# Kernel tuning notes

Measured on AMD Instinct MI355X. Metric: run time of the kernel, lower is better.

Reference implementation:

```python
import jax, jax.numpy as jnp
import numpy as np
import math

SQRT2 = float(np.sqrt(2.0))
INV_SQRT_2PI = float(1.0 / np.sqrt(2.0 * np.pi))


def _trunc_prob(x, mu, sigma):
    # Faithful port of TruncNormal.prob with a=-10, b=10
    a, b = -10.0, 10.0
    phi_b = 0.5 * (1.0 + jax.scipy.special.erf((b - mu) / sigma / SQRT2))
    phi_a = 0.5 * (1.0 + jax.scipy.special.erf((a - mu) / sigma / SQRT2))
    xs = jnp.where(x > b, x + 100.0, x)
    xs = jnp.where(xs < a, xs - 100.0, xs)
    xn = (xs - mu) / sigma
    dens = jnp.exp(-0.5 * xn * xn) * INV_SQRT_2PI
    dens = jnp.where((xn > b) | (xn < a), 0.0, dens)
    return dens / (phi_b - phi_a) + 1e-10


def _S_single(zg, tt, Wx, bx, Wt, bt, Wt2, bt2, Wf, bf, Wo, bo):
    # One tiny MLP applied to one group-slice zg (shape [g]) at scalar time tt.
    g = Wx.shape[0]
    x = jnp.tanh(Wx @ zg + bx)
    half = g // 2
    freqs = jnp.exp(jnp.arange(half, dtype=zg.dtype) * (-math.log(10000.0) / half))
    te = tt * freqs
    temb = jnp.concatenate([jnp.sin(te), jnp.cos(te)])  # [g]
    tv = jax.nn.gelu(Wt @ temb + bt, approximate=False)  # torch nn.GELU (exact)
    tv = Wt2 @ tv + bt2
    h = jnp.tanh(Wf @ (x + tv) + bf)
    return jnp.tanh(Wo @ h + bo)[0]  # scalar S


def _derivs(zg, tt, Wx, bx, Wt, bt, Wt2, bt2, Wf, bf, Wo, bo):
    p = (Wx, bx, Wt, bt, Wt2, bt2, Wf, bf, Wo, bo)
    f = lambda z_, t_: _S_single(z_, t_, *p)
    S = f(zg, tt)
    s_z = jax.grad(f, 0)(zg, tt)                    # dS/dz         [g]
    H = jax.jacfwd(jax.grad(f, 0), 0)(zg, tt)       # H[j,k]=d2S/dzj dzk  [g,g]
    dSdt = jax.grad(f, 1)(zg, tt)                   # dS/dt scalar
    return S, s_z, H, dSdt


def reference(z, time_step, mu, sigma, Wx, bx, Wt, bt, Wt2, bt2, Wf, bf, Wo, bo, beta):
    G, g = Wx.shape[0], Wx.shape[1]
    B = z.shape[0]
    tt = time_step[0]

    sig2 = sigma ** 2 + 1e-5
    nlp = -(z - mu) / sig2                                   # nabla_log_phi [B,n_in]
    dlp = -1.0 / sig2                                        # delta_log_phi (scalar-ish)
    dpp = ((z - mu) ** 2 - sigma ** 2) / (sigma ** 4 + 1e-5)  # delta_phi_over_phi
    rho = _trunc_prob(z, mu, sigma)

    to_g = lambda a: a.reshape(B, G, g).transpose(1, 0, 2)   # [G,B,g]
    zr, nlp_r, dpp_r, rho_r = to_g(z), to_g(nlp), to_g(dpp), to_g(rho)

    over_b = jax.vmap(_derivs, in_axes=(0, None) + (None,) * 10)
    over_g = jax.vmap(over_b, in_axes=(0, None) + (0,) * 10)
    S, s_z, H, dSdt = over_g(zr, tt, Wx, bx, Wt, bt, Wt2, bt2, Wf, bf, Wo, bo)
    # S [G,B], s_z [G,B,g], H [G,B,g,g], dSdt [G,B]

    bb = beta.reshape(G, 1, 1)
    u = S[..., None] - bb * jnp.log(jnp.prod(rho_r, axis=2, keepdims=True))  # [G,B,1]
    u_z = s_z - bb * nlp_r                                                    # [G,B,g]
    # torch grad(S.sum(), t): t is a single shared (1,1) tensor -> gradient sums over batch
    dSdt_sum = dSdt.sum(axis=1).reshape(G, 1, 1)
    # grad((rho*u_z).sum(), z_temp): rho and nabla_log_phi are constants wrt z_temp,
    # so gradient = sum_j rho_j * H[j,k]
    corr = jnp.einsum('gbj,gbjk->gbk', rho_r, H)
    u_t = dSdt_sum + bb * corr / (rho_r + 1e-5)
    # grad(s_z.sum(), z_temp)[k] = sum_j H[j,k]
    u_zz = H.sum(axis=2) - bb * dlp
    pde = u_t + 0.5 * u_z ** 2 + 0.125 * bb ** 2 * (nlp_r ** 2 - 2.0 * dpp_r)

    to_bn = lambda a: a.transpose(1, 0, 2).reshape(B, -1)
    return to_bn(pde), to_bn(u_z), u[:, :, 0].transpose(1, 0), to_bn(u_zz)


def setup_inputs() -> dict:
    B, N_IN, g = 8192, 512, 4
    G = N_IN // g
    key = jax.random.key(0)
    ks = jax.random.split(key, 16)

    def lin_w(k, fo, fi):
        return (jax.random.normal(k, (G, fo, fi), jnp.float32) / np.sqrt(fi)).astype(jnp.float32)

    def lin_b(k, fo):
        return (0.01 * jax.random.normal(k, (G, fo), jnp.float32)).astype(jnp.float32)

    return {
        "z": jax.random.normal(ks[0], (B, N_IN), jnp.float32),
        "time_step": jnp.ones((1,), jnp.float32),
        "mu": jnp.zeros((1,), jnp.float32),
        "sigma": jnp.ones((1,), jnp.float32),
        "Wx": lin_w(ks[1], g, g), "bx": lin_b(ks[2], g),
        "Wt": lin_w(ks[3], g, g), "bt": lin_b(ks[4], g),
        "Wt2": lin_w(ks[5], g, g), "bt2": lin_b(ks[6], g),
        "Wf": lin_w(ks[7], g, g), "bf": lin_b(ks[8], g),
        "Wo": lin_w(ks[9], 1, g), "bo": lin_b(ks[10], 1),
        "beta": jnp.ones((G, 1), jnp.float32),
    }
```

## Files before the change

kernel.cpp:

```cpp
#include <hip/hip_runtime.h>
#include <math.h>

#define NG 128
#define NIN 512
#define OFF1 4194304
#define OFF2 8388608
#define OFF3 9437184

#define INV_SQRT_2PI 0.3989422804014327f
#define INV_SQRT2    0.7071067811865476f

__device__ __forceinline__ float gelu_f(float x){
    return 0.5f*x*(1.0f + erff(x*INV_SQRT2));
}
__device__ __forceinline__ float gelu_df(float x){
    return 0.5f*(1.0f + erff(x*INV_SQRT2)) + x*INV_SQRT_2PI*expf(-0.5f*x*x);
}

__global__ void k_pre(const float* __restrict__ ts,
                      const float* __restrict__ Wt,  const float* __restrict__ bt,
                      const float* __restrict__ Wt2, const float* __restrict__ bt2,
                      float* __restrict__ tv_ws, float* __restrict__ dtv_ws){
    int g = threadIdx.x;
    if (g >= NG) return;
    float t  = ts[0];
    float f1 = expf(-0.5f*logf(10000.0f));
    float te0 = t, te1 = t*f1;
    float temb[4]  = { sinf(te0),  sinf(te1),     cosf(te0),     cosf(te1) };
    float dtemb[4] = { cosf(te0),  f1*cosf(te1), -sinf(te0), -f1*sinf(te1) };
    float tg[4], dg[4];
    #pragma unroll
    for (int i=0;i<4;i++){
        float a = bt[g*4+i], d = 0.0f;
        #pragma unroll
        for (int j=0;j<4;j++){
            float w = Wt[g*16+i*4+j];
            a += w*temb[j]; d += w*dtemb[j];
        }
        tg[i] = gelu_f(a);
        dg[i] = gelu_df(a)*d;
    }
    #pragma unroll
    for (int j=0;j<4;j++){
        float a = bt2[g*4+j], d = 0.0f;
        #pragma unroll
        for (int i=0;i<4;i++){
            float w = Wt2[g*16+j*4+i];
            a += w*tg[i]; d += w*dg[i];
        }
        tv_ws[g*4+j]  = a;
        dtv_ws[g*4+j] = d;
    }
}

__global__ __launch_bounds__(256) void k_dsdt(const float* __restrict__ z,
    const float* __restrict__ Wx, const float* __restrict__ bx,
    const float* __restrict__ Wf, const float* __restrict__ bf,
    const float* __restrict__ Wo, const float* __restrict__ bo,
    const float* __restrict__ tv_ws, const float* __restrict__ dtv_ws,
    float* __restrict__ partial){
    const int tid  = threadIdx.x;
    const int gidx = tid & 127;
    const int lb   = tid >> 7;
    float wx[16], wf[16];
    #pragma unroll
    for (int i=0;i<4;i++){
        float4 a4 = ((const float4*)(Wx + gidx*16))[i];
        wx[i*4+0]=a4.x; wx[i*4+1]=a4.y; wx[i*4+2]=a4.z; wx[i*4+3]=a4.w;
        float4 b4 = ((const float4*)(Wf + gidx*16))[i];
        wf[i*4+0]=b4.x; wf[i*4+1]=b4.y; wf[i*4+2]=b4.z; wf[i*4+3]=b4.w;
    }
    float4 t4;
    t4 = ((const float4*)bx)[gidx];     float bxA[4]={t4.x,t4.y,t4.z,t4.w};
    t4 = ((const float4*)bf)[gidx];     float bfA[4]={t4.x,t4.y,t4.z,t4.w};
    t4 = ((const float4*)Wo)[gidx];     float w3[4] ={t4.x,t4.y,t4.z,t4.w};
    t4 = ((const float4*)tv_ws)[gidx];  float tvA[4]={t4.x,t4.y,t4.z,t4.w};
    t4 = ((const float4*)dtv_ws)[gidx]; float dtvA[4]={t4.x,t4.y,t4.z,t4.w};
    float bo0 = bo[gidx];

    float acc = 0.0f;
    const int b0 = blockIdx.x*16 + lb;
    #pragma unroll
    for (int k=0;k<8;k++){
        int b = b0 + 2*k;
        float4 zv = *((const float4*)(z + b*NIN + gidx*4));
        float zz[4]={zv.x,zv.y,zv.z,zv.w};
        float u1[4];
        #pragma unroll
        for (int i=0;i<4;i++){
            float a = bxA[i] + wx[i*4]*zz[0]+wx[i*4+1]*zz[1]+wx[i*4+2]*zz[2]+wx[i*4+3]*zz[3];
            float x = tanhf(a);
            u1[i] = x + tvA[i];
        }
        float hp[4];
        float a3 = bo0;
        #pragma unroll
        for (int i=0;i<4;i++){
            float a = bfA[i] + wf[i*4]*u1[0]+wf[i*4+1]*u1[1]+wf[i*4+2]*u1[2]+wf[i*4+3]*u1[3];
            float h = tanhf(a);
            hp[i] = 1.0f - h*h;
            a3 += w3[i]*h;
        }
        float S = tanhf(a3), sp = 1.0f - S*S;
        float q[4]={0.f,0.f,0.f,0.f};
        #pragma unroll
        for (int i=0;i<4;i++){
            float vi = sp*w3[i]*hp[i];
            #pragma unroll
            for (int j=0;j<4;j++) q[j] += vi*wf[i*4+j];
        }
        acc += q[0]*dtvA[0]+q[1]*dtvA[1]+q[2]*dtvA[2]+q[3]*dtvA[3];
    }
    __shared__ float sred[256];
    sred[tid] = acc;
    __syncthreads();
    if (tid < 128) partial[tid*512 + blockIdx.x] = sred[tid] + sred[tid+128];
}

__global__ void k_red(const float* __restrict__ partial, float* __restrict__ dsum){
    int g = blockIdx.x;
    int t = threadIdx.x;
    float a = 0.0f;
    for (int i=t;i<512;i+=64) a += partial[g*512+i];
    #pragma unroll
    for (int o=32;o>0;o>>=1) a += __shfl_down(a, o);
    if (t==0) dsum[g] = a;
}

__global__ __launch_bounds__(256) void k_main(const float* __restrict__ z,
    const float* __restrict__ mup, const float* __restrict__ sigp,
    const float* __restrict__ Wx, const float* __restrict__ bx,
    const float* __restrict__ Wf, const float* __restrict__ bf,
    const float* __restrict__ Wo, const float* __restrict__ bo,
    const float* __restrict__ betap, const float* __restrict__ tv_ws,
    const float* __restrict__ dsum, float* __restrict__ out){
    const int tid  = threadIdx.x;
    const int gidx = tid & 127;
    const int b    = blockIdx.x*2 + (tid>>7);

    const float mu = mup[0], sigma = sigp[0];
    const float sig2   = sigma*sigma + 1e-5f;
    const float dlp    = -1.0f/sig2;
    const float inv_s4 = 1.0f/(sigma*sigma*sigma*sigma + 1e-5f);
    const float phi_b  = 0.5f*(1.0f+erff((10.0f-mu)/sigma*INV_SQRT2));
    const float phi_a  = 0.5f*(1.0f+erff((-10.0f-mu)/sigma*INV_SQRT2));
    const float invZ   = 1.0f/(phi_b-phi_a);

    float wx[16], wf[16];
    #pragma unroll
    for (int i=0;i<4;i++){
        float4 a4 = ((const float4*)(Wx + gidx*16))[i];
        wx[i*4+0]=a4.x; wx[i*4+1]=a4.y; wx[i*4+2]=a4.z; wx[i*4+3]=a4.w;
        float4 b4 = ((const float4*)(Wf + gidx*16))[i];
        wf[i*4+0]=b4.x; wf[i*4+1]=b4.y; wf[i*4+2]=b4.z; wf[i*4+3]=b4.w;
    }
    float4 t4;
    t4 = ((const float4*)bx)[gidx];    float bxA[4]={t4.x,t4.y,t4.z,t4.w};
    t4 = ((const float4*)bf)[gidx];    float bfA[4]={t4.x,t4.y,t4.z,t4.w};
    t4 = ((const float4*)Wo)[gidx];    float w3[4] ={t4.x,t4.y,t4.z,t4.w};
    t4 = ((const float4*)tv_ws)[gidx]; float tvA[4]={t4.x,t4.y,t4.z,t4.w};
    const float bo0    = bo[gidx];
    const float bb     = betap[gidx];
    const float dS_sum = dsum[gidx];

    float4 zv = *((const float4*)(z + b*NIN + gidx*4));
    float zz[4]={zv.x,zv.y,zv.z,zv.w};

    float x[4], xp[4], u1[4];
    #pragma unroll
    for (int i=0;i<4;i++){
        float a = bxA[i] + wx[i*4]*zz[0]+wx[i*4+1]*zz[1]+wx[i*4+2]*zz[2]+wx[i*4+3]*zz[3];
        x[i] = tanhf(a); xp[i] = 1.0f - x[i]*x[i];
        u1[i] = x[i] + tvA[i];
    }
    float h[4], hp[4];
    float a3 = bo0;
    #pragma unroll
    for (int i=0;i<4;i++){
        float a = bfA[i] + wf[i*4]*u1[0]+wf[i*4+1]*u1[1]+wf[i*4+2]*u1[2]+wf[i*4+3]*u1[3];
        h[i] = tanhf(a); hp[i] = 1.0f - h[i]*h[i];
        a3 += w3[i]*h[i];
    }
    float S = tanhf(a3), sp = 1.0f - S*S;

    float Bm[16];
    #pragma unroll
    for (int i=0;i<4;i++){
        #pragma unroll
        for (int n=0;n<4;n++){
            float s = 0.0f;
            #pragma unroll
            for (int k=0;k<4;k++) s += wf[i*4+k]*xp[k]*wx[k*4+n];
            Bm[i*4+n]=s;
        }
    }
    float w3hp[4], v[4];
    #pragma unroll
    for (int i=0;i<4;i++){ w3hp[i]=w3[i]*hp[i]; v[i]=sp*w3hp[i]; }
    float q[4]={0.f,0.f,0.f,0.f};
    #pragma unroll
    for (int i=0;i<4;i++){
        #pragma unroll
        for (int j=0;j<4;j++) q[j] += v[i]*wf[i*4+j];
    }
    float c[4];
    #pragma unroll
    for (int n=0;n<4;n++){
        float s=0.0f;
        #pragma unroll
        for (int i=0;i<4;i++) s += w3hp[i]*Bm[i*4+n];
        c[n]=s;
    }
    const float alpha = -2.0f*S*sp;
    float bet[4], gam[4];
    #pragma unroll
    for (int i=0;i<4;i++){ bet[i] = -2.0f*h[i]*v[i]; gam[i] = -2.0f*x[i]*xp[i]*q[i]; }

    float rho[4], nlp[4], dpp[4];
    #pragma unroll
    for (int j=0;j<4;j++){
        float zj = zz[j];
        float xs = zj > 10.0f ? zj+100.0f : zj;
        xs = xs < -10.0f ? xs-100.0f : xs;
        float xn = (xs-mu)/sigma;
        float dens = expf(-0.5f*xn*xn)*INV_SQRT_2PI;
        dens = (xn > 10.0f || xn < -10.0f) ? 0.0f : dens;
        rho[j] = dens*invZ + 1e-10f;
        nlp[j] = -(zj-mu)/sig2;
        float d = zj-mu;
        dpp[j] = (d*d - sigma*sigma)*inv_s4;
    }
    float u_val = S - bb*logf(rho[0]*rho[1]*rho[2]*rho[3]);

    float rc=0.0f, scs=0.0f;
    #pragma unroll
    for (int j=0;j<4;j++){ rc += rho[j]*c[j]; scs += c[j]; }
    float rB[4], sB[4], rA[4], sA[4];
    #pragma unroll
    for (int i=0;i<4;i++){
        float r=0.0f, s=0.0f, r2=0.0f, s2=0.0f;
        #pragma unroll
        for (int j=0;j<4;j++){
            r  += rho[j]*Bm[i*4+j]; s  += Bm[i*4+j];
            r2 += rho[j]*wx[i*4+j]; s2 += wx[i*4+j];
        }
        rB[i]=r; sB[i]=s; rA[i]=r2; sA[i]=s2;
    }

    float pde[4], uz[4], uzz[4];
    #pragma unroll
    for (int k=0;k<4;k++){
        float corr = alpha*rc*c[k];
        float hsum = alpha*scs*c[k];
        #pragma unroll
        for (int i=0;i<4;i++){
            corr += bet[i]*rB[i]*Bm[i*4+k];
            hsum += bet[i]*sB[i]*Bm[i*4+k];
            corr += gam[i]*rA[i]*wx[i*4+k];
            hsum += gam[i]*sA[i]*wx[i*4+k];
        }
        float uzk = sp*c[k] - bb*nlp[k];
        float utk = dS_sum + bb*corr/(rho[k]+1e-5f);
        uz[k]  = uzk;
        uzz[k] = hsum - bb*dlp;
        pde[k] = utk + 0.5f*uzk*uzk + 0.125f*bb*bb*(nlp[k]*nlp[k] - 2.0f*dpp[k]);
    }

    const int base = b*NIN + gidx*4;
    *((float4*)(out + base))        = make_float4(pde[0],pde[1],pde[2],pde[3]);
    *((float4*)(out + OFF1 + base)) = make_float4(uz[0],uz[1],uz[2],uz[3]);
    out[OFF2 + b*NG + gidx] = u_val;
    *((float4*)(out + OFF3 + base)) = make_float4(uzz[0],uzz[1],uzz[2],uzz[3]);
}

extern "C" void kernel_launch(void* const* d_in, const int* in_sizes, int n_in,
                              void* d_out, int out_size, void* d_ws, size_t ws_size,
                              hipStream_t stream){
    (void)in_sizes; (void)n_in; (void)out_size; (void)ws_size;
    const float* z     = (const float*)d_in[0];
    const float* ts    = (const float*)d_in[1];
    const float* mu    = (const float*)d_in[2];
    const float* sigma = (const float*)d_in[3];
    const float* Wx    = (const float*)d_in[4];
    const float* bx    = (const float*)d_in[5];
    const float* Wt    = (const float*)d_in[6];
    const float* bt    = (const float*)d_in[7];
    const float* Wt2   = (const float*)d_in[8];
    const float* bt2   = (const float*)d_in[9];
    const float* Wf    = (const float*)d_in[10];
    const float* bf    = (const float*)d_in[11];
    const float* Wo    = (const float*)d_in[12];
    const float* bo    = (const float*)d_in[13];
    const float* beta  = (const float*)d_in[14];
    float* out = (float*)d_out;

    float* ws      = (float*)d_ws;
    float* tv_ws   = ws;
    float* dtv_ws  = ws + 512;
    float* dsum    = ws + 1024;
    float* partial = ws + 1152;

    k_pre <<<1,   128, 0, stream>>>(ts, Wt, bt, Wt2, bt2, tv_ws, dtv_ws);
    k_dsdt<<<512, 256, 0, stream>>>(z, Wx, bx, Wf, bf, Wo, bo, tv_ws, dtv_ws, partial);
    k_red <<<128,  64, 0, stream>>>(partial, dsum);
    k_main<<<4096,256, 0, stream>>>(z, mu, sigma, Wx, bx, Wf, bf, Wo, bo, beta, tv_ws, dsum, out);
}
```

Baseline: 147.7 us.

## Use fast tanh/exp/rcp intrinsics, precompute scalar constants, and widen dS/dt grid

Replaces tanhf with an exp+rcp based tanh, swaps divisions and expf/logf for fast intrinsics, and moves the per-thread sigma/mu constant computation (erf, divides) into the one-block pre-kernel. The dS/dt partial kernel now runs on four times as many blocks with fewer rows each, and the partial layout and reduction kernel are changed to match. The fast math lowers transcendental cost but gives up accuracy, and the exp-based tanh may overflow for large arguments.

```diff
diff --git a/kernel.cpp b/kernel.cpp
--- a/kernel.cpp
+++ b/kernel.cpp
@@ -10,6 +10,13 @@
 #define INV_SQRT_2PI 0.3989422804014327f
 #define INV_SQRT2    0.7071067811865476f
 
+__device__ __forceinline__ float ftanh(float x){
+    float e = __expf(2.0f*x);
+    float r = __builtin_amdgcn_rcpf(e + 1.0f);
+    return 1.0f - 2.0f*r;
+}
+__device__ __forceinline__ float frcp(float x){ return __builtin_amdgcn_rcpf(x); }
+
 __device__ __forceinline__ float gelu_f(float x){
     return 0.5f*x*(1.0f + erff(x*INV_SQRT2));
 }
@@ -18,10 +25,25 @@
 }
 
 __global__ void k_pre(const float* __restrict__ ts,
+                      const float* __restrict__ mup, const float* __restrict__ sigp,
                       const float* __restrict__ Wt,  const float* __restrict__ bt,
                       const float* __restrict__ Wt2, const float* __restrict__ bt2,
-                      float* __restrict__ tv_ws, float* __restrict__ dtv_ws){
+                      float* __restrict__ tv_ws, float* __restrict__ dtv_ws,
+                      float* __restrict__ consts){
     int g = threadIdx.x;
+    if (g == 0){
+        float mu = mup[0], sigma = sigp[0];
+        float sig2   = sigma*sigma + 1e-5f;
+        float phi_b  = 0.5f*(1.0f+erff((10.0f-mu)/sigma*INV_SQRT2));
+        float phi_a  = 0.5f*(1.0f+erff((-10.0f-mu)/sigma*INV_SQRT2));
+        consts[0] = sig2;
+        consts[1] = -1.0f/sig2;
+        consts[2] = 1.0f/(sigma*sigma*sigma*sigma + 1e-5f);
+        consts[3] = 1.0f/(phi_b-phi_a);
+        consts[4] = mu;
+        consts[5] = 1.0f/sigma;
+        consts[6] = sigma;
+    }
     if (g >= NG) return;
     float t  = ts[0];
     float f1 = expf(-0.5f*logf(10000.0f));
@@ -79,9 +101,9 @@
     float bo0 = bo[gidx];
 
     float acc = 0.0f;
-    const int b0 = blockIdx.x*16 + lb;
-    #pragma unroll
-    for (int k=0;k<8;k++){
+    const int b0 = blockIdx.x*4 + lb;
+    #pragma unroll
+    for (int k=0;k<2;k++){
         int b = b0 + 2*k;
         float4 zv = *((const float4*)(z + b*NIN + gidx*4));
         float zz[4]={zv.x,zv.y,zv.z,zv.w};
@@ -89,19 +111,18 @@
         #pragma unroll
         for (int i=0;i<4;i++){
             float a = bxA[i] + wx[i*4]*zz[0]+wx[i*4+1]*zz[1]+wx[i*4+2]*zz[2]+wx[i*4+3]*zz[3];
-            float x = tanhf(a);
-            u1[i] = x + tvA[i];
+            u1[i] = ftanh(a) + tvA[i];
         }
         float hp[4];
         float a3 = bo0;
         #pragma unroll
         for (int i=0;i<4;i++){
             float a = bfA[i] + wf[i*4]*u1[0]+wf[i*4+1]*u1[1]+wf[i*4+2]*u1[2]+wf[i*4+3]*u1[3];
-            float h = tanhf(a);
+            float h = ftanh(a);
             hp[i] = 1.0f - h*h;
             a3 += w3[i]*h;
         }
-        float S = tanhf(a3), sp = 1.0f - S*S;
+        float S = ftanh(a3), sp = 1.0f - S*S;
         float q[4]={0.f,0.f,0.f,0.f};
         #pragma unroll
         for (int i=0;i<4;i++){
@@ -114,37 +135,45 @@
     __shared__ float sred[256];
     sred[tid] = acc;
     __syncthreads();
-    if (tid < 128) partial[tid*512 + blockIdx.x] = sred[tid] + sred[tid+128];
-}
-
-__global__ void k_red(const float* __restrict__ partial, float* __restrict__ dsum){
+    if (tid < 128) partial[blockIdx.x*128 + tid] = sred[tid] + sred[tid+128];
+}
+
+__global__ __launch_bounds__(256) void k_red(const float* __restrict__ partial,
+                                             float* __restrict__ dsum){
     int g = blockIdx.x;
-    int t = threadIdx.x;
+    int tid = threadIdx.x;
     float a = 0.0f;
-    for (int i=t;i<512;i+=64) a += partial[g*512+i];
-    #pragma unroll
-    for (int o=32;o>0;o>>=1) a += __shfl_down(a, o);
-    if (t==0) dsum[g] = a;
+    for (int i=tid;i<2048;i+=256) a += partial[i*128+g];
+    __shared__ float s[256];
+    s[tid] = a;
+    __syncthreads();
+    if (tid < 64){
+        a = s[tid] + s[tid+64] + s[tid+128] + s[tid+192];
+        #pragma unroll
+        for (int o=32;o>0;o>>=1) a += __shfl_down(a, o);
+        if (tid==0) dsum[g] = a;
+    }
 }
 
 __global__ __launch_bounds__(256) void k_main(const float* __restrict__ z,
-    const float* __restrict__ mup, const float* __restrict__ sigp,
     const float* __restrict__ Wx, const float* __restrict__ bx,
     const float* __restrict__ Wf, const float* __restrict__ bf,
     const float* __restrict__ Wo, const float* __restrict__ bo,
     const float* __restrict__ betap, const float* __restrict__ tv_ws,
+    const float* __restrict__ consts,
     const float* __restrict__ dsum, float* __restrict__ out){
     const int tid  = threadIdx.x;
     const int gidx = tid & 127;
     const int b    = blockIdx.x*2 + (tid>>7);
 
-    const float mu = mup[0], sigma = sigp[0];
-    const float sig2   = sigma*sigma + 1e-5f;
-    const float dlp    = -1.0f/sig2;
-    const float inv_s4 = 1.0f/(sigma*sigma*sigma*sigma + 1e-5f);
-    const float phi_b  = 0.5f*(1.0f+erff((10.0f-mu)/sigma*INV_SQRT2));
-    const float phi_a  = 0.5f*(1.0f+erff((-10.0f-mu)/sigma*INV_SQRT2));
-    const float invZ   = 1.0f/(phi_b-phi_a);
+    const float sig2    = consts[0];
+    const float dlp     = consts[1];
+    const float inv_s4  = consts[2];
+    const float invZ    = consts[3];
+    const float mu      = consts[4];
+    const float inv_sig = consts[5];
+    const float sigma   = consts[6];
+    const float inv_sig2 = frcp(sig2);
 
     float wx[16], wf[16];
     #pragma unroll
@@ -170,7 +199,7 @@
     #pragma unroll
     for (int i=0;i<4;i++){
         float a = bxA[i] + wx[i*4]*zz[0]+wx[i*4+1]*zz[1]+wx[i*4+2]*zz[2]+wx[i*4+3]*zz[3];
-        x[i] = tanhf(a); xp[i] = 1.0f - x[i]*x[i];
+        x[i] = ftanh(a); xp[i] = 1.0f - x[i]*x[i];
         u1[i] = x[i] + tvA[i];
     }
     float h[4], hp[4];
@@ -178,10 +207,10 @@
     #pragma unroll
     for (int i=0;i<4;i++){
         float a = bfA[i] + wf[i*4]*u1[0]+wf[i*4+1]*u1[1]+wf[i*4+2]*u1[2]+wf[i*4+3]*u1[3];
-        h[i] = tanhf(a); hp[i] = 1.0f - h[i]*h[i];
+        h[i] = ftanh(a); hp[i] = 1.0f - h[i]*h[i];
         a3 += w3[i]*h[i];
     }
-    float S = tanhf(a3), sp = 1.0f - S*S;
+    float S = ftanh(a3), sp = 1.0f - S*S;
 
     float Bm[16];
     #pragma unroll
@@ -222,15 +251,15 @@
         float zj = zz[j];
         float xs = zj > 10.0f ? zj+100.0f : zj;
         xs = xs < -10.0f ? xs-100.0f : xs;
-        float xn = (xs-mu)/sigma;
-        float dens = expf(-0.5f*xn*xn)*INV_SQRT_2PI;
+        float xn = (xs-mu)*inv_sig;
+        float dens = __expf(-0.5f*xn*xn)*INV_SQRT_2PI;
         dens = (xn > 10.0f || xn < -10.0f) ? 0.0f : dens;
         rho[j] = dens*invZ + 1e-10f;
-        nlp[j] = -(zj-mu)/sig2;
+        nlp[j] = -(zj-mu)*inv_sig2;
         float d = zj-mu;
         dpp[j] = (d*d - sigma*sigma)*inv_s4;
     }
-    float u_val = S - bb*logf(rho[0]*rho[1]*rho[2]*rho[3]);
+    float u_val = S - bb*__logf(rho[0]*rho[1]*rho[2]*rho[3]);
 
     float rc=0.0f, scs=0.0f;
     #pragma unroll
@@ -260,7 +289,7 @@
             hsum += gam[i]*sA[i]*wx[i*4+k];
         }
         float uzk = sp*c[k] - bb*nlp[k];
-        float utk = dS_sum + bb*corr/(rho[k]+1e-5f);
+        float utk = dS_sum + bb*corr*frcp(rho[k]+1e-5f);
         uz[k]  = uzk;
         uzz[k] = hsum - bb*dlp;
         pde[k] = utk + 0.5f*uzk*uzk + 0.125f*bb*bb*(nlp[k]*nlp[k] - 2.0f*dpp[k]);
@@ -297,11 +326,12 @@
     float* ws      = (float*)d_ws;
     float* tv_ws   = ws;
     float* dtv_ws  = ws + 512;
-    float* dsum    = ws + 1024;
-    float* partial = ws + 1152;
-
-    k_pre <<<1,   128, 0, stream>>>(ts, Wt, bt, Wt2, bt2, tv_ws, dtv_ws);
-    k_dsdt<<<512, 256, 0, stream>>>(z, Wx, bx, Wf, bf, Wo, bo, tv_ws, dtv_ws, partial);
-    k_red <<<128,  64, 0, stream>>>(partial, dsum);
-    k_main<<<4096,256, 0, stream>>>(z, mu, sigma, Wx, bx, Wf, bf, Wo, bo, beta, tv_ws, dsum, out);
-}
+    float* consts  = ws + 1024;
+    float* dsum    = ws + 1032;
+    float* partial = ws + 1160;
+
+    k_pre <<<1,   128, 0, stream>>>(ts, mu, sigma, Wt, bt, Wt2, bt2, tv_ws, dtv_ws, consts);
+    k_dsdt<<<2048,256, 0, stream>>>(z, Wx, bx, Wf, bf, Wo, bo, tv_ws, dtv_ws, partial);
+    k_red <<<128, 256, 0, stream>>>(partial, dsum);
+    k_main<<<4096,256, 0, stream>>>(z, Wx, bx, Wf, bf, Wo, bo, beta, tv_ws, consts, dsum, out);
+}
```

After: 131.0 us. 11.3% less time.
